# Kernel tuning notes

Hardware: AMD Instinct MI355X
Metric: run time of the kernel (lower is better)

## Reference

```python
import jax, jax.numpy as jnp
import numpy as np

NUM_CLASSES = 33  # labels 0..32; class 0 = background, 32 instances
EPS = 1e-06


def _lovasz_hinge_flat(logits, labels):
    # logits, labels: flat 1-D float arrays (labels in {0,1})
    signs = 2.0 * labels - 1.0
    errors = 1.0 - logits * signs
    order = jnp.argsort(-errors)            # descending sort
    errors_sorted = errors[order]
    gt_sorted = labels[order]
    gts = jnp.sum(gt_sorted)
    intersection = gts - jnp.cumsum(gt_sorted)
    union = gts + jnp.cumsum(1.0 - gt_sorted)
    jaccard = 1.0 - intersection / union
    grad = jnp.concatenate([jaccard[:1], jaccard[1:] - jaccard[:-1]])
    return jnp.dot(jax.nn.relu(errors_sorted), grad)


def _per_sample_loss(y_emb, y_sig, gt_patch):
    # y_emb: [2,H,W] float, y_sig: [1,H,W] float, gt_patch: [1,H,W] int
    # to_onehot(gt)[0, 1:] -> [N,H,W], N = NUM_CLASSES-1 instance channels
    gt_one_hot = jax.nn.one_hot(gt_patch[0], NUM_CLASSES, axis=0, dtype=y_emb.dtype)[1:]
    counts = jnp.sum(gt_one_hot, axis=(1, 2), keepdims=True)          # [N,1,1]
    # per-instance embedding centers: [2,N,1,1]
    centers = jnp.sum(gt_one_hot[None] * y_emb[:, None], axis=(2, 3), keepdims=True) / counts
    instance_sigmas = gt_one_hot[None] * y_sig[:, None]               # [1,N,H,W]
    sigmas = jnp.sum(instance_sigmas, axis=(2, 3), keepdims=True) / counts  # [1,N,1,1]
    var_sigmas = jnp.sum(((instance_sigmas - jax.lax.stop_gradient(sigmas)) * gt_one_hot) ** 2) / counts  # [N,1,1]
    center_dist = jnp.linalg.norm(centers - y_emb[:, None], axis=0)   # [N,H,W]
    probs = jnp.exp(-0.5 * (center_dist / sigmas) ** 2)               # [1,N,H,W]
    logits = (probs * 2.0 - 1.0).reshape(-1)
    labels = jnp.broadcast_to(gt_one_hot[None], probs.shape).reshape(-1)
    return _lovasz_hinge_flat(logits, labels) + jnp.mean(var_sigmas)


def setup_inputs() -> dict:
    key = jax.random.key(0)
    k1, k2, k3 = jax.random.split(key, 3)
    B, H, W = 4, 512, 512
    y_embeddings = jax.random.normal(k1, (B, 2, H, W), dtype=jnp.float32)
    y_sigma = jax.random.uniform(k2, (B, 1, H, W), dtype=jnp.float32)
    y_true = jax.random.randint(k3, (B, 1, H, W), 0, NUM_CLASSES, dtype=jnp.int64)
    return {"y_embeddings": y_embeddings, "y_sigma": y_sigma, "y_true": y_true}


def reference(y_embeddings, y_sigma, y_true):
    # Assumes every sample contains foreground (random labels over 512x512
    # guarantee this w.h.p.), so the torch `if torch.any(gt>0)` branch is taken
    # for all samples and the final loss is the mean over the batch.
    losses = jax.vmap(_per_sample_loss)(y_embeddings, y_sigma, y_true)
    return jnp.mean(losses)
```

## Files before the change

kernel.cpp:

```cpp
#include <hip/hip_runtime.h>

#define HW    262144
#define BNUM  4
#define NC    33
#define NI    32

#define NB     1024
#define BSCALE 64.0f
#define EG     4096
#define ESCALE 2048.0f

typedef unsigned long long ull;

#define W_CNTC 0
#define W_CNTF 4
#define W_FINL 8
#define W_VART 12
#define W_EGRID 16
#define W_HIST  (W_EGRID + BNUM * 2 * EG)
#define W_PART  (W_HIST + BNUM * 128 * NB)
#define PJ 168
#define PS (128 * PJ)

__global__ void __launch_bounds__(256) stats_kernel(
    const float* __restrict__ emb, const float* __restrict__ sig,
    const int* __restrict__ gt, float* __restrict__ ws) {
  int s = blockIdx.y;
  int j = blockIdx.x;
  int t = threadIdx.x;
  int w = t >> 6;
  __shared__ float acc[4][165];
  int bid = s * 128 + j;
  unsigned* wsu = (unsigned*)ws;
  if (t < 64) wsu[W_EGRID + bid * 64 + t] = 0u;
  if (bid == 0 && t < 16) wsu[t] = 0u;
  for (int k = t; k < 4 * 165; k += 256) ((float*)acc)[k] = 0.f;
  __syncthreads();
  const float* e0p = emb + (size_t)s * 2 * HW;
  const float* e1p = e0p + HW;
  const float* sp  = sig + (size_t)s * HW;
  const int*   gp  = gt  + (size_t)s * HW;
  #pragma unroll
  for (int i = 0; i < 2; ++i) {
    int idx = j * 2048 + i * 1024 + t * 4;
    int4   lb = *(const int4*)(gp + idx);
    float4 x  = *(const float4*)(e0p + idx);
    float4 y  = *(const float4*)(e1p + idx);
    float4 sg = *(const float4*)(sp + idx);
#define ACC(L, X, Y, SG)                                                   \
    if (L > 0) {                                                           \
      atomicAdd(&acc[w][L], X);        atomicAdd(&acc[w][33 + L], Y);      \
      atomicAdd(&acc[w][66 + L], SG);  atomicAdd(&acc[w][99 + L], (SG)*(SG)); \
      atomicAdd(&acc[w][132 + L], 1.0f);                                   \
    }
    ACC(lb.x, x.x, y.x, sg.x)
    ACC(lb.y, x.y, y.y, sg.y)
    ACC(lb.z, x.z, y.z, sg.z)
    ACC(lb.w, x.w, y.w, sg.w)
#undef ACC
  }
  __syncthreads();
  if (t < 165) {
    float v = acc[0][t] + acc[1][t] + acc[2][t] + acc[3][t];
    ws[W_PART + s * PS + j * PJ + t] = v;
  }
}

__global__ void __launch_bounds__(512) hist_kernel(
    const float* __restrict__ emb, const int* __restrict__ gt,
    float* __restrict__ ws) {
  int s  = blockIdx.y;
  int lb = blockIdx.x;
  int t = threadIdx.x;
  int lane = t & 63, wid = t >> 6;
  __shared__ unsigned hist[NB * 8];
  __shared__ float sums2[2][165];
  __shared__ float sums[165];
  __shared__ float4 cons[NC];
  for (int k = t; k < NB * 8; k += 512) hist[k] = 0u;
  if (t < 330) {
    int r = (t >= 165) ? 1 : 0;
    int c = t - r * 165;
    const float* pp = ws + W_PART + s * PS + (r << 6) * PJ + c;
    float sum = 0.f;
    #pragma unroll 16
    for (int jj = 0; jj < 64; ++jj) sum += pp[jj * PJ];
    sums2[r][c] = sum;
  }
  __syncthreads();
  if (t < 165) sums[t] = sums2[0][t] + sums2[1][t];
  __syncthreads();
  if (t >= 1 && t < NC) {
    float c = sums[132 + t];
    float4 C;
    if (c > 0.f) {
      float inv = 1.0f / c;
      float c0 = sums[t] * inv, c1 = sums[33 + t] * inv, sgm = sums[66 + t] * inv;
      float Q = 0.5f / (sgm * sgm) * BSCALE;
      C.x = Q; C.y = -2.0f * Q * c0; C.z = -2.0f * Q * c1;
      C.w = Q * (c0 * c0 + c1 * c1);
    } else {
      C.x = 0.f; C.y = 0.f; C.z = 0.f; C.w = (float)NB;
    }
    cons[t] = C;
  }
  if (lb == 0 && wid == 0) {
    float S = 0.f, rcp = 0.f;
    if (lane >= 1 && lane < NC) {
      float c = sums[132 + lane];
      if (c > 0.f) {
        float sg = sums[66 + lane] / c;
        S = sums[99 + lane] - c * sg * sg;
        rcp = 1.0f / c;
      }
    }
    for (int o = 32; o; o >>= 1) {
      S   += __shfl_down(S, o);
      rcp += __shfl_down(rcp, o);
    }
    if (lane == 0) ws[W_VART + s] = S * rcp / (float)NI;
  }
  __syncthreads();
  const float* e0p = emb + (size_t)s * 2 * HW;
  const float* e1p = e0p + HW;
  const int*   gp  = gt  + (size_t)s * HW;
  int idx = lb * 2048 + t * 4;
  int4   lbl = *(const int4*)(gp + idx);
  float4 px  = *(const float4*)(e0p + idx);
  float4 py  = *(const float4*)(e1p + idx);
  float4 ss;
  ss.x = fmaf(px.x, px.x, py.x * py.x);
  ss.y = fmaf(px.y, px.y, py.y * py.y);
  ss.z = fmaf(px.z, px.z, py.z * py.z);
  ss.w = fmaf(px.w, px.w, py.w * py.w);
  unsigned* hr = hist + (t & 7);
#define POSFIX(P0, P1, SV, L)                                            \
    if (L > 0) {                                                         \
      float4 C = cons[L];                                                \
      float bf = fmaf(C.x, SV, fmaf(C.y, P0, fmaf(C.z, P1, C.w)));       \
      int ib = min((int)bf, NB - 1);                                     \
      atomicAdd(&hr[ib << 3], 0xFFFFu);                                  \
    }
  POSFIX(px.x, py.x, ss.x, lbl.x)
  POSFIX(px.y, py.y, ss.y, lbl.y)
  POSFIX(px.z, py.z, ss.z, lbl.z)
  POSFIX(px.w, py.w, ss.w, lbl.w)
#undef POSFIX
  #pragma unroll 4
  for (int n = 1; n <= NI; ++n) {
    float4 C = cons[n];
#define ITEM(P0, P1, SV)                                               \
    {                                                                  \
      float bf = fmaf(C.x, SV, fmaf(C.y, P0, fmaf(C.z, P1, C.w)));     \
      int ib = min((int)bf, NB - 1);                                   \
      atomicAdd(&hr[ib << 3], 1u);                                     \
    }
    ITEM(px.x, py.x, ss.x)
    ITEM(px.y, py.y, ss.y)
    ITEM(px.z, py.z, ss.z)
    ITEM(px.w, py.w, ss.w)
#undef ITEM
  }
  __syncthreads();
  unsigned* gh = (unsigned*)ws + W_HIST + s * (128 * NB);
  for (int k = t; k < NB; k += 512) {
    uint4 a = *(uint4*)&hist[k * 8];
    uint4 b = *(uint4*)&hist[k * 8 + 4];
    gh[k * 128 + lb] = a.x + a.y + a.z + a.w + b.x + b.y + b.z + b.w;
  }
}

__global__ void __launch_bounds__(512) merge_scan_kernel(
    float* __restrict__ ws, float* __restrict__ out) {
  int s  = blockIdx.y;
  int lb = blockIdx.x;
  int t = threadIdx.x;
  int lane = t & 63, wid = t >> 6;
  __shared__ unsigned eg[EG * 2];
  __shared__ ull wsum[8];
  __shared__ float red[8];
  __shared__ int flag;
  unsigned* gh = (unsigned*)ws + W_HIST + s * (128 * NB);
  int b = lb * 8 + wid;
  unsigned v0 = gh[b * 128 + lane];
  unsigned v1 = gh[b * 128 + 64 + lane];
  ull pv = ((ull)((v0 >> 16) + (v1 >> 16)) << 32)
         | (ull)((v0 & 0xFFFFu) + (v1 & 0xFFFFu));
  for (int o = 32; o; o >>= 1) pv += __shfl_down(pv, o);
  if (lane == 0) {
    unsigned pos = (unsigned)(pv >> 32), neg = (unsigned)(pv & 0xFFFFFFFFu);
    unsigned* egp = (unsigned*)ws + W_EGRID + s * 2 * EG;
    unsigned* egn = egp + EG;
    float tc = ((float)b + 0.5f) * (1.0f / BSCALE);
    float ex = __expf(-tc);
    if (pos) {
      float e = 2.0f - 2.0f * ex;
      int k = (int)(e * ESCALE); if (k > EG - 1) k = EG - 1;
      atomicAdd(&egp[k], pos);
    }
    if (neg) {
      float e = 2.0f * ex;
      int k = (int)(e * ESCALE); if (k > EG - 1) k = EG - 1;
      atomicAdd(&egn[k], neg);
    }
  }
  __syncthreads();
  if (t == 0) {
    __threadfence();
    flag = (atomicAdd((unsigned*)ws + W_CNTC + s, 1u) == 127u);
  }
  __syncthreads();
  if (!flag) return;

  __threadfence();
  unsigned* egg = (unsigned*)ws + W_EGRID + s * 2 * EG;
  for (int k = t; k < 2 * EG; k += 512) eg[k] = egg[k];
  float vart = ws[W_VART + s];
  __syncthreads();
  unsigned* ep = eg;
  unsigned* en = eg + EG;
  const int CH = EG / 512;
  int j0 = t * CH;
  unsigned np = 0, nn = 0;
  for (int k = 0; k < CH; ++k) {
    int bb = EG - 1 - (j0 + k);
    np += ep[bb]; nn += en[bb];
  }
  ull v = ((ull)np << 32) | (ull)nn;
  ull inc = v;
  for (int o = 1; o < 64; o <<= 1) {
    ull u = __shfl_up(inc, o);
    if (lane >= o) inc += u;
  }
  if (lane == 63) wsum[wid] = inc;
  __syncthreads();
  ull offset = 0, total = 0;
  for (int i = 0; i < 8; ++i) {
    ull xr = wsum[i];
    if (i < wid) offset += xr;
    total += xr;
  }
  ull excl = offset + inc - v;
  float P = (float)(unsigned)(total >> 32);
  unsigned p = (unsigned)(excl >> 32), f = (unsigned)(excl & 0xFFFFFFFFu);
  float jprev = 1.0f - (P - (float)p) / (P + (float)f);
  float contrib = 0.f;
  for (int k = 0; k < CH; ++k) {
    int bb = EG - 1 - (j0 + k);
    unsigned ap_ = ep[bb], an_ = en[bb];
    if (ap_ | an_) {
      p += ap_; f += an_;
      float j = 1.0f - (P - (float)p) / (P + (float)f);
      float e = ((float)bb + 0.5f) * (2.0f / EG);
      contrib += e * (j - jprev);
      jprev = j;
    }
  }
  for (int o = 32; o; o >>= 1) contrib += __shfl_down(contrib, o);
  if (lane == 0) red[wid] = contrib;
  __syncthreads();
  if (t == 0) {
    float tot = 0.f;
    for (int i = 0; i < 8; ++i) tot += red[i];
    float loss = tot + vart;
    float* fin = ws + W_FINL;
    atomicExch(&fin[s], loss);
    __threadfence();
    unsigned old = atomicAdd((unsigned*)ws + W_CNTF, 1u);
    if (old == BNUM - 1) {
      float a = 0.f;
      for (int i = 0; i < BNUM; ++i) a += atomicAdd(&fin[i], 0.0f);
      out[0] = a * (1.0f / BNUM);
    }
  }
}

extern "C" void kernel_launch(void* const* d_in, const int* in_sizes, int n_in,
                              void* d_out, int out_size, void* d_ws, size_t ws_size,
                              hipStream_t stream) {
  const float* emb = (const float*)d_in[0];
  const float* sig = (const float*)d_in[1];
  const int*   gt  = (const int*)d_in[2];
  float* out = (float*)d_out;
  float* ws  = (float*)d_ws;

  dim3 g(128, BNUM);
  stats_kernel<<<g, 256, 0, stream>>>(emb, sig, gt, ws);
  hist_kernel<<<g, 512, 0, stream>>>(emb, gt, ws);
  merge_scan_kernel<<<g, 512, 0, stream>>>(ws, out);
}
```

Before: 129.7 us.

## Fuse histogram and merge-scan kernels using a last-block-per-sample reduction

Merges the histogram kernel and the merge/scan kernel into one launch. Each block writes its partial histogram to global memory, then the last block to arrive for a sample merges all 128 partial histograms into an LDS error grid and runs the Lovasz scan there. This removes one kernel launch, the global error-grid buffer with its zeroing and global atomics, and the separate variance-term handoff through workspace. In exchange, the cross-block merge that used to be spread over 128 blocks now runs serially in a single block per sample, which lengthens the tail.

```diff
diff --git a/kernel.cpp b/kernel.cpp
--- a/kernel.cpp
+++ b/kernel.cpp
@@ -15,10 +15,8 @@
 #define W_CNTC 0
 #define W_CNTF 4
 #define W_FINL 8
-#define W_VART 12
-#define W_EGRID 16
-#define W_HIST  (W_EGRID + BNUM * 2 * EG)
-#define W_PART  (W_HIST + BNUM * 128 * NB)
+#define W_HIST 16
+#define W_PART (W_HIST + BNUM * 128 * NB)
 #define PJ 168
 #define PS (128 * PJ)
 
@@ -32,7 +30,6 @@
   __shared__ float acc[4][165];
   int bid = s * 128 + j;
   unsigned* wsu = (unsigned*)ws;
-  if (t < 64) wsu[W_EGRID + bid * 64 + t] = 0u;
   if (bid == 0 && t < 16) wsu[t] = 0u;
   for (int k = t; k < 4 * 165; k += 256) ((float*)acc)[k] = 0.f;
   __syncthreads();
@@ -66,9 +63,9 @@
   }
 }
 
-__global__ void __launch_bounds__(512) hist_kernel(
+__global__ void __launch_bounds__(512) hist_merge_scan_kernel(
     const float* __restrict__ emb, const int* __restrict__ gt,
-    float* __restrict__ ws) {
+    float* __restrict__ ws, float* __restrict__ out) {
   int s  = blockIdx.y;
   int lb = blockIdx.x;
   int t = threadIdx.x;
@@ -77,6 +74,10 @@
   __shared__ float sums2[2][165];
   __shared__ float sums[165];
   __shared__ float4 cons[NC];
+  __shared__ ull wsum[8];
+  __shared__ float red[8];
+  __shared__ float vart_s;
+  __shared__ int flag;
   for (int k = t; k < NB * 8; k += 512) hist[k] = 0u;
   if (t < 330) {
     int r = (t >= 165) ? 1 : 0;
@@ -103,22 +104,6 @@
       C.x = 0.f; C.y = 0.f; C.z = 0.f; C.w = (float)NB;
     }
     cons[t] = C;
-  }
-  if (lb == 0 && wid == 0) {
-    float S = 0.f, rcp = 0.f;
-    if (lane >= 1 && lane < NC) {
-      float c = sums[132 + lane];
-      if (c > 0.f) {
-        float sg = sums[66 + lane] / c;
-        S = sums[99 + lane] - c * sg * sg;
-        rcp = 1.0f / c;
-      }
-    }
-    for (int o = 32; o; o >>= 1) {
-      S   += __shfl_down(S, o);
-      rcp += __shfl_down(rcp, o);
-    }
-    if (lane == 0) ws[W_VART + s] = S * rcp / (float)NI;
   }
   __syncthreads();
   const float* e0p = emb + (size_t)s * 2 * HW;
@@ -168,42 +153,6 @@
     uint4 b = *(uint4*)&hist[k * 8 + 4];
     gh[k * 128 + lb] = a.x + a.y + a.z + a.w + b.x + b.y + b.z + b.w;
   }
-}
-
-__global__ void __launch_bounds__(512) merge_scan_kernel(
-    float* __restrict__ ws, float* __restrict__ out) {
-  int s  = blockIdx.y;
-  int lb = blockIdx.x;
-  int t = threadIdx.x;
-  int lane = t & 63, wid = t >> 6;
-  __shared__ unsigned eg[EG * 2];
-  __shared__ ull wsum[8];
-  __shared__ float red[8];
-  __shared__ int flag;
-  unsigned* gh = (unsigned*)ws + W_HIST + s * (128 * NB);
-  int b = lb * 8 + wid;
-  unsigned v0 = gh[b * 128 + lane];
-  unsigned v1 = gh[b * 128 + 64 + lane];
-  ull pv = ((ull)((v0 >> 16) + (v1 >> 16)) << 32)
-         | (ull)((v0 & 0xFFFFu) + (v1 & 0xFFFFu));
-  for (int o = 32; o; o >>= 1) pv += __shfl_down(pv, o);
-  if (lane == 0) {
-    unsigned pos = (unsigned)(pv >> 32), neg = (unsigned)(pv & 0xFFFFFFFFu);
-    unsigned* egp = (unsigned*)ws + W_EGRID + s * 2 * EG;
-    unsigned* egn = egp + EG;
-    float tc = ((float)b + 0.5f) * (1.0f / BSCALE);
-    float ex = __expf(-tc);
-    if (pos) {
-      float e = 2.0f - 2.0f * ex;
-      int k = (int)(e * ESCALE); if (k > EG - 1) k = EG - 1;
-      atomicAdd(&egp[k], pos);
-    }
-    if (neg) {
-      float e = 2.0f * ex;
-      int k = (int)(e * ESCALE); if (k > EG - 1) k = EG - 1;
-      atomicAdd(&egn[k], neg);
-    }
-  }
   __syncthreads();
   if (t == 0) {
     __threadfence();
@@ -213,12 +162,49 @@
   if (!flag) return;
 
   __threadfence();
-  unsigned* egg = (unsigned*)ws + W_EGRID + s * 2 * EG;
-  for (int k = t; k < 2 * EG; k += 512) eg[k] = egg[k];
-  float vart = ws[W_VART + s];
-  __syncthreads();
-  unsigned* ep = eg;
-  unsigned* en = eg + EG;
+  for (int k = t; k < 2 * EG; k += 512) hist[k] = 0u;
+  if (wid == 0) {
+    float S = 0.f, rcp = 0.f;
+    if (lane >= 1 && lane < NC) {
+      float c = sums[132 + lane];
+      if (c > 0.f) {
+        float sg = sums[66 + lane] / c;
+        S = sums[99 + lane] - c * sg * sg;
+        rcp = 1.0f / c;
+      }
+    }
+    for (int o = 32; o; o >>= 1) {
+      S   += __shfl_down(S, o);
+      rcp += __shfl_down(rcp, o);
+    }
+    if (lane == 0) vart_s = S * rcp / (float)NI;
+  }
+  __syncthreads();
+  unsigned* ep = hist;
+  unsigned* en = hist + EG;
+  #pragma unroll 16
+  for (int bb = wid; bb < NB; bb += 8) {
+    const uint2 v = *(const uint2*)&gh[bb * 128 + lane * 2];
+    ull pv = ((ull)((v.x >> 16) + (v.y >> 16)) << 32)
+           | (ull)((v.x & 0xFFFFu) + (v.y & 0xFFFFu));
+    for (int o = 32; o; o >>= 1) pv += __shfl_down(pv, o);
+    if (lane == 0 && pv) {
+      unsigned pos = (unsigned)(pv >> 32), neg = (unsigned)pv;
+      float tc = ((float)bb + 0.5f) * (1.0f / BSCALE);
+      float ex = __expf(-tc);
+      if (pos) {
+        float e = 2.0f - 2.0f * ex;
+        int k = (int)(e * ESCALE); if (k > EG - 1) k = EG - 1;
+        atomicAdd(&ep[k], pos);
+      }
+      if (neg) {
+        float e = 2.0f * ex;
+        int k = (int)(e * ESCALE); if (k > EG - 1) k = EG - 1;
+        atomicAdd(&en[k], neg);
+      }
+    }
+  }
+  __syncthreads();
   const int CH = EG / 512;
   int j0 = t * CH;
   unsigned np = 0, nn = 0;
@@ -262,7 +248,7 @@
   if (t == 0) {
     float tot = 0.f;
     for (int i = 0; i < 8; ++i) tot += red[i];
-    float loss = tot + vart;
+    float loss = tot + vart_s;
     float* fin = ws + W_FINL;
     atomicExch(&fin[s], loss);
     __threadfence();
@@ -286,6 +272,5 @@
 
   dim3 g(128, BNUM);
   stats_kernel<<<g, 256, 0, stream>>>(emb, sig, gt, ws);
-  hist_kernel<<<g, 512, 0, stream>>>(emb, gt, ws);
-  merge_scan_kernel<<<g, 512, 0, stream>>>(ws, out);
+  hist_merge_scan_kernel<<<g, 512, 0, stream>>>(emb, gt, ws, out);
 }
```

New measurement: 214.8 us. 1.66x slower.
